# Performance work log

Hardware: AMD Instinct MI355X
Metric: run time of the kernel (lower is better)

## Reference

```python
import jax, jax.numpy as jnp
import numpy as np

B, T, D, H = 4, 2048, 1024, 16
HD = D // H  # 64
EPS = 1e-5

def _layernorm(x, g, b):
    mu = jnp.mean(x, axis=-1, keepdims=True)
    var = jnp.var(x, axis=-1, keepdims=True)
    return (x - mu) * jax.lax.rsqrt(var + EPS) * g + b

def setup_inputs() -> dict:
    key = jax.random.key(0)
    ks = jax.random.split(key, 8)
    s = D ** -0.5
    return {
        "x":  jax.random.normal(ks[0], (B, T, D), jnp.float32),
        "Wq": jax.random.normal(ks[1], (H, D, HD), jnp.float32) * s,
        "Wk": jax.random.normal(ks[2], (H, D, HD), jnp.float32) * s,
        "Wv": jax.random.normal(ks[3], (H, D, HD), jnp.float32) * s,
        "Wp": jax.random.normal(ks[4], (D, D), jnp.float32) * s,
        "bp": jnp.zeros((D,), jnp.float32),
        "W1": jax.random.normal(ks[5], (D, 4 * D), jnp.float32) * s,
        "b1": jnp.zeros((4 * D,), jnp.float32),
        "W2": jax.random.normal(ks[6], (4 * D, D), jnp.float32) * (4 * D) ** -0.5,
        "b2": jnp.zeros((D,), jnp.float32),
        "g1": jnp.ones((D,), jnp.float32),
        "be1": jnp.zeros((D,), jnp.float32),
        "g2": jnp.ones((D,), jnp.float32),
        "be2": jnp.zeros((D,), jnp.float32),
    }

def reference(x, Wq, Wk, Wv, Wp, bp, W1, b1, W2, b2, g1, be1, g2, be2):
    # --- pre-LN causal MHA (all heads batched; torch code loops per head) ---
    h = _layernorm(x, g1, be1)                       # [B,T,D]
    q = jnp.einsum('btd,hdk->bhtk', h, Wq)
    k = jnp.einsum('btd,hdk->bhtk', h, Wk)
    v = jnp.einsum('btd,hdk->bhtk', h, Wv)
    scores = jnp.einsum('bhtk,bhsk->bhts', q, k) * (HD ** -0.5)
    causal = jnp.tril(jnp.ones((T, T), bool))
    scores = jnp.where(causal, scores, -jnp.inf)
    w = jax.nn.softmax(scores, axis=-1)              # [B,H,T,T]
    o = jnp.einsum('bhts,bhsk->bhtk', w, v)          # [B,H,T,HD]
    o = o.transpose(0, 2, 1, 3).reshape(x.shape[0], x.shape[1], D)  # concat heads
    x = x + o @ Wp + bp                              # residual 1
    # --- pre-LN FFN ---
    h2 = _layernorm(x, g2, be2)
    ff = jax.nn.relu(h2 @ W1 + b1) @ W2 + b2
    return x + ff
```

## Files before the change

kernel.cpp:

```cpp
#include <hip/hip_runtime.h>
#include <hip/hip_bf16.h>
#include <math.h>

#define Bsz 4
#define Tsz 2048
#define Dsz 1024
#define Hn  16
#define HDs 64

typedef __attribute__((ext_vector_type(8))) short bf16x8;
typedef __attribute__((ext_vector_type(4))) float f32x4;

typedef const __attribute__((address_space(1))) void gvoid;
typedef __attribute__((address_space(3))) void lvoid;

__device__ __forceinline__ void async_copy16(const short* g, short* l) {
    __builtin_amdgcn_global_load_lds((gvoid*)g, (lvoid*)l, 16, 0, 0);
}

__device__ __forceinline__ short f2bf(float x) {
    __hip_bfloat16 h = __float2bfloat16(x);
    return *reinterpret_cast<short*>(&h);
}

__device__ __forceinline__ unsigned int pack_bf16(float hi, float lo) {
    unsigned int uh = __float_as_uint(hi) + 0x8000u;
    unsigned int ul = __float_as_uint(lo) + 0x8000u;
    return __builtin_amdgcn_perm(uh, ul, 0x07060302u);
}

__device__ __forceinline__ size_t headed_idx(int m, int c) {
    int b = m >> 11, t = m & 2047, h = c >> 6, kc = c & 63;
    return (((size_t)(b * Hn + h) * Tsz + t) << 6) + kc;
}

__global__ __launch_bounds__(256) void ln_kernel(const float* __restrict__ x,
                                                 const float* __restrict__ g,
                                                 const float* __restrict__ beta,
                                                 short* __restrict__ out)
{
    const int row = blockIdx.x;
    const float* xr = x + (size_t)row * Dsz;
    float v[4];
    float s = 0.f, s2 = 0.f;
#pragma unroll
    for (int i = 0; i < 4; ++i) {
        v[i] = xr[threadIdx.x + 256 * i];
        s += v[i];
        s2 += v[i] * v[i];
    }
#pragma unroll
    for (int off = 32; off; off >>= 1) {
        s  += __shfl_xor(s,  off);
        s2 += __shfl_xor(s2, off);
    }
    __shared__ float red[8];
    const int wave = threadIdx.x >> 6;
    if ((threadIdx.x & 63) == 0) { red[wave * 2] = s; red[wave * 2 + 1] = s2; }
    __syncthreads();
    s  = red[0] + red[2] + red[4] + red[6];
    s2 = red[1] + red[3] + red[5] + red[7];
    const float mu  = s * (1.f / Dsz);
    const float var = s2 * (1.f / Dsz) - mu * mu;
    const float rs  = rsqrtf(var + 1e-5f);
    short* orow = out + (size_t)row * Dsz;
#pragma unroll
    for (int i = 0; i < 4; ++i) {
        int col = threadIdx.x + 256 * i;
        orow[col] = f2bf((v[i] - mu) * rs * g[col] + beta[col]);
    }
}

__global__ __launch_bounds__(256) void transpose_cvt(
    const float* __restrict__ in, short* __restrict__ outp, int R, int C)
{
    __shared__ float tile[32][33];
    const int r0 = blockIdx.y * 32, c0 = blockIdx.x * 32;
    const size_t so = (size_t)blockIdx.z * R * C;
    const int tx = threadIdx.x & 31, ty = threadIdx.x >> 5;
    const float* ip = in + so;
    short* op = outp + so;
#pragma unroll
    for (int i = 0; i < 4; ++i)
        tile[ty + i * 8][tx] = ip[(size_t)(r0 + ty + i * 8) * C + c0 + tx];
    __syncthreads();
#pragma unroll
    for (int i = 0; i < 4; ++i)
        op[(size_t)(c0 + ty + i * 8) * R + r0 + tx] = f2bf(tile[tx][ty + i * 8]);
}

__global__ __launch_bounds__(256) void transpose_cvt_qkv(
    const float* __restrict__ Wq, const float* __restrict__ Wk,
    const float* __restrict__ Wv, short* __restrict__ outp)
{
    __shared__ float tile[32][33];
    const int z = blockIdx.z;
    const float* in = (z < 16) ? Wq : (z < 32) ? Wk : Wv;
    const int zz = z & 15;
    const int r0 = blockIdx.y * 32, c0 = blockIdx.x * 32;
    const int tx = threadIdx.x & 31, ty = threadIdx.x >> 5;
    const float* ip = in + (size_t)zz * (1024 * 64);
    short* op = outp + (size_t)z * (1024 * 64);
#pragma unroll
    for (int i = 0; i < 4; ++i)
        tile[ty + i * 8][tx] = ip[(size_t)(r0 + ty + i * 8) * 64 + c0 + tx];
    __syncthreads();
#pragma unroll
    for (int i = 0; i < 4; ++i)
        op[(size_t)(c0 + ty + i * 8) * 1024 + r0 + tx] = f2bf(tile[tx][ty + i * 8]);
}

template <int EPI>
__global__ __launch_bounds__(256) void gemm_mfma(
    const short* __restrict__ A, const short* __restrict__ Bt,
    const float* __restrict__ bias, const float* __restrict__ resid,
    float* __restrict__ Cf, short* __restrict__ Cb0,
    short* __restrict__ Cb1, short* __restrict__ Cb2,
    int M, int N, int K, float scale)
{
    __shared__ short As[2][128 * 32];
    __shared__ short Bs[2][128 * 32];
    const int tid  = threadIdx.x;
    const int lane = tid & 63, wave = tid >> 6;
    const int quad = lane >> 4, l16 = lane & 15;

    const int lin = blockIdx.y * gridDim.x + blockIdx.x;
    const int xcd = lin & 7;
    const int s   = lin >> 3;
    const int my  = xcd * 8 + (s & 7);
    const int nx  = s >> 3;
    const int m0 = my * 128, n0 = nx * 128;

    const int wm = (wave >> 1) * 64, wn = (wave & 1) * 64;

    f32x4 acc[4][4];
#pragma unroll
    for (int i = 0; i < 4; ++i)
#pragma unroll
        for (int j = 0; j < 4; ++j) acc[i][j] = f32x4{0.f, 0.f, 0.f, 0.f};

    const short* gA = A  + (size_t)(m0 + wave * 32 + (lane >> 2)) * K + (lane & 3) * 8;
    const short* gB = Bt + (size_t)(n0 + wave * 32 + (lane >> 2)) * K + (lane & 3) * 8;
    const size_t rstep = (size_t)16 * K;
    const int woff = wave * 1024;

    auto stageg = [&](int buf) {
        async_copy16(gA,         &As[buf][woff]);
        async_copy16(gA + rstep, &As[buf][woff + 512]);
        async_copy16(gB,         &Bs[buf][woff]);
        async_copy16(gB + rstep, &Bs[buf][woff + 512]);
        gA += 32; gB += 32;
    };

    stageg(0);
    stageg(1);

    const int ntile = K >> 5;
    int cur = 0;
    for (int t = 0; t < ntile; ++t) {
        if (t + 1 < ntile) asm volatile("s_waitcnt vmcnt(4)" ::: "memory");
        else               asm volatile("s_waitcnt vmcnt(0)" ::: "memory");
        __builtin_amdgcn_s_barrier();
        __builtin_amdgcn_sched_barrier(0);

        bf16x8 af[4], bfr[4];
#pragma unroll
        for (int mt = 0; mt < 4; ++mt)
            af[mt] = *(const bf16x8*)(&As[cur][(wm + mt * 16 + l16) * 32 + quad * 8]);
#pragma unroll
        for (int nt2 = 0; nt2 < 4; ++nt2)
            bfr[nt2] = *(const bf16x8*)(&Bs[cur][(wn + nt2 * 16 + l16) * 32 + quad * 8]);

        if (t + 2 < ntile) {
            asm volatile("s_waitcnt lgkmcnt(0)" ::: "memory");
            __builtin_amdgcn_sched_barrier(0);
            __builtin_amdgcn_s_barrier();
            __builtin_amdgcn_sched_barrier(0);
            stageg(cur);
        }

#pragma unroll
        for (int mt = 0; mt < 4; ++mt)
#pragma unroll
            for (int nt2 = 0; nt2 < 4; ++nt2)
                acc[mt][nt2] = __builtin_amdgcn_mfma_f32_16x16x32_bf16(
                    af[mt], bfr[nt2], acc[mt][nt2], 0, 0, 0);
        cur ^= 1;
    }

#pragma unroll
    for (int mt = 0; mt < 4; ++mt) {
#pragma unroll
        for (int nt2 = 0; nt2 < 4; ++nt2) {
#pragma unroll
            for (int r = 0; r < 4; ++r) {
                const int m = m0 + wm + mt * 16 + quad * 4 + r;
                const int c = n0 + wn + nt2 * 16 + l16;
                float val = acc[mt][nt2][r];
                if (EPI == 0) {
                    const int sel = c >> 10, cl = c & 1023;
                    if (sel == 0)
                        Cb0[headed_idx(m, cl)] = f2bf(val * scale);
                    else if (sel == 1)
                        Cb1[headed_idx(m, cl)] = f2bf(val);
                    else {
                        int b = m >> 11, t = m & 2047;
                        size_t idx = ((((size_t)((b << 4) | (cl >> 6)) << 6) | (cl & 63)) << 11) | t;
                        Cb2[idx] = f2bf(val);
                    }
                } else if (EPI == 2) {
                    size_t idx = (size_t)m * N + c;
                    Cf[idx] = val + bias[c] + resid[idx];
                } else {
                    float v2 = val + bias[c];
                    Cb0[(size_t)m * N + c] = f2bf(v2 > 0.f ? v2 : 0.f);
                }
            }
        }
    }
}

__global__ __launch_bounds__(256) void gemm_n64(
    const short* __restrict__ A, const short* __restrict__ Bt,
    const float* __restrict__ bias, const float* __restrict__ resid,
    float* __restrict__ Cf, int M, int N, int K)
{
    __shared__ short As[2][128 * 64];
    __shared__ short Bs[2][64 * 64];
    const int tid  = threadIdx.x;
    const int lane = tid & 63, wave = tid >> 6;
    const int quad = lane >> 4, l16 = lane & 15;

    const int lin = blockIdx.y * 16 + blockIdx.x;
    const int xcd = lin & 7;
    const int s   = lin >> 3;
    const int m0  = (xcd * 8 + (s & 7)) * 128;
    const int n0  = (s >> 3) * 64;

    const int wm = (wave >> 1) * 64, wn = (wave & 1) * 32;

    f32x4 acc[4][2];
#pragma unroll
    for (int i = 0; i < 4; ++i)
#pragma unroll
        for (int j = 0; j < 2; ++j) acc[i][j] = f32x4{0.f, 0.f, 0.f, 0.f};

    const short* gA[4];
    const short* gB[2];
    int dA[4], dB[2];
#pragma unroll
    for (int i = 0; i < 4; ++i) {
        const int sl = tid + 256 * i, r = sl >> 3, g = (sl & 7) ^ (r & 7);
        gA[i] = A + (size_t)(m0 + r) * K + g * 8;
        dA[i] = sl * 8;
    }
#pragma unroll
    for (int i = 0; i < 2; ++i) {
        const int sl = tid + 256 * i, r = sl >> 3, g = (sl & 7) ^ (r & 7);
        gB[i] = Bt + (size_t)(n0 + r) * K + g * 8;
        dB[i] = sl * 8;
    }

    auto stageg = [&](int buf) {
#pragma unroll
        for (int i = 0; i < 4; ++i) { async_copy16(gA[i], &As[buf][dA[i]]); gA[i] += 64; }
#pragma unroll
        for (int i = 0; i < 2; ++i) { async_copy16(gB[i], &Bs[buf][dB[i]]); gB[i] += 64; }
    };

    stageg(0);
    stageg(1);

    const int ntile = K >> 6;
    int cur = 0;
    for (int t = 0; t < ntile; ++t) {
        if (t + 1 < ntile) asm volatile("s_waitcnt vmcnt(6)" ::: "memory");
        else               asm volatile("s_waitcnt vmcnt(0)" ::: "memory");
        __builtin_amdgcn_s_barrier();
        __builtin_amdgcn_sched_barrier(0);

        bf16x8 af[4][2], bfr[2][2];
#pragma unroll
        for (int mt = 0; mt < 4; ++mt) {
            const int r = wm + mt * 16 + l16;
            af[mt][0] = *(const bf16x8*)(&As[cur][r * 64 + (((quad    ) ^ (r & 7)) << 3)]);
            af[mt][1] = *(const bf16x8*)(&As[cur][r * 64 + (((quad + 4) ^ (r & 7)) << 3)]);
        }
#pragma unroll
        for (int nt2 = 0; nt2 < 2; ++nt2) {
            const int r = wn + nt2 * 16 + l16;
            bfr[nt2][0] = *(const bf16x8*)(&Bs[cur][r * 64 + (((quad    ) ^ (r & 7)) << 3)]);
            bfr[nt2][1] = *(const bf16x8*)(&Bs[cur][r * 64 + (((quad + 4) ^ (r & 7)) << 3)]);
        }

        if (t + 2 < ntile) {
            asm volatile("s_waitcnt lgkmcnt(0)" ::: "memory");
            __builtin_amdgcn_sched_barrier(0);
            __builtin_amdgcn_s_barrier();
            __builtin_amdgcn_sched_barrier(0);
            stageg(cur);
        }

#pragma unroll
        for (int mt = 0; mt < 4; ++mt)
#pragma unroll
            for (int nt2 = 0; nt2 < 2; ++nt2) {
                acc[mt][nt2] = __builtin_amdgcn_mfma_f32_16x16x32_bf16(
                    af[mt][0], bfr[nt2][0], acc[mt][nt2], 0, 0, 0);
                acc[mt][nt2] = __builtin_amdgcn_mfma_f32_16x16x32_bf16(
                    af[mt][1], bfr[nt2][1], acc[mt][nt2], 0, 0, 0);
            }
        cur ^= 1;
    }

#pragma unroll
    for (int mt = 0; mt < 4; ++mt) {
#pragma unroll
        for (int nt2 = 0; nt2 < 2; ++nt2) {
#pragma unroll
            for (int r = 0; r < 4; ++r) {
                const int m = m0 + wm + mt * 16 + quad * 4 + r;
                const int c = n0 + wn + nt2 * 16 + l16;
                const size_t idx = (size_t)m * N + c;
                Cf[idx] = acc[mt][nt2][r] + bias[c] + resid[idx];
            }
        }
    }
}

__global__ __launch_bounds__(256, 4) void fattn_kernel(
    const short* __restrict__ Q,
    const short* __restrict__ K,
    const short* __restrict__ VT,
    short* __restrict__ O)
{
    __shared__ short Kl[2][64 * 64];
    __shared__ short Vl[2][64 * 64];
    __shared__ short p_lds[4][16 * 64];
    const int tid  = threadIdx.x;
    const int lane = tid & 63, wave = tid >> 6;
    const int quad = lane >> 4, l16 = lane & 15;

    const int lin  = blockIdx.y * 16 + blockIdx.x;
    const int xcd  = lin & 7;
    const int slot = lin >> 3;
    const int bh   = xcd * 8 + (slot >> 4);
    const int px   = slot & 15;
    const int tiles[2] = { 31 - px, px };

    const int bb = bh >> 4, hh = bh & 15;
    const size_t bhoff = (size_t)bh * (Tsz * HDs);
    const short* Qb = Q + bhoff;
    const short* Kb = K + bhoff;
    const short* Vb = VT + bhoff;

    const int s_a = tid, s_b = tid + 256;
    const int ra = s_a >> 3, ga = (s_a & 7) ^ (ra & 7);
    const int rb = s_b >> 3, gb = (s_b & 7) ^ (rb & 7);

    short* pw = &p_lds[wave][0];
    const int rd0 = l16 * 64 + (((quad    ) ^ (l16 & 7)) << 3);
    const int rd1 = l16 * 64 + (((quad + 4) ^ (l16 & 7)) << 3);

    bf16x8 bq[2][2];
#pragma unroll
    for (int ti = 0; ti < 2; ++ti) {
        const short* qp = Qb + (size_t)(tiles[ti] * 64 + wave * 16 + l16) * 64 + quad * 8;
        bq[ti][0] = *(const bf16x8*)qp;
        bq[ti][1] = *(const bf16x8*)(qp + 32);
    }

    auto stage = [&](int c64, int buf) {
        short* kb_l = &Kl[buf][0];
        short* vb_l = &Vl[buf][0];
        async_copy16(Kb + (((size_t)(c64 + ra)) << 6) + (ga << 3), kb_l + s_a * 8);
        async_copy16(Kb + (((size_t)(c64 + rb)) << 6) + (gb << 3), kb_l + s_b * 8);
        async_copy16(Vb + ((size_t)ra << 11) + c64 + (ga << 3), vb_l + s_a * 8);
        async_copy16(Vb + ((size_t)rb << 11) + c64 + (gb << 3), vb_l + s_b * 8);
    };

    stage(tiles[0] * 0, 0);
    __syncthreads();

    int phase = 0;
#pragma unroll
    for (int ti = 0; ti < 2; ++ti) {
        const int tile = tiles[ti];
        const int q0w  = tile * 64 + wave * 16;
        const int nch  = tile + 1;

        f32x4 oaccT[4];
        float lacc = 0.f;
#pragma unroll
        for (int nt = 0; nt < 4; ++nt) oaccT[nt] = f32x4{0.f, 0.f, 0.f, 0.f};

        for (int c = 0; c < nch; ++c) {
            const int cur = phase & 1;
            if (c + 1 < nch)   stage((c + 1) * 64, cur ^ 1);
            else if (ti == 0)  stage(0, cur ^ 1);

            const int s0 = c * 64;
            const short* Kc = &Kl[cur][0];
            const short* Vc = &Vl[cur][0];
            bf16x8 ak[4][2], av[4][2];
#pragma unroll
            for (int ct = 0; ct < 4; ++ct) {
                const int r = ct * 16 + l16;
                ak[ct][0] = *(const bf16x8*)(Kc + r * 64 + (((quad    ) ^ (r & 7)) << 3));
                ak[ct][1] = *(const bf16x8*)(Kc + r * 64 + (((quad + 4) ^ (r & 7)) << 3));
            }
#pragma unroll
            for (int nt = 0; nt < 4; ++nt) {
                const int r = nt * 16 + l16;
                av[nt][0] = *(const bf16x8*)(Vc + r * 64 + (((quad    ) ^ (r & 7)) << 3));
                av[nt][1] = *(const bf16x8*)(Vc + r * 64 + (((quad + 4) ^ (r & 7)) << 3));
            }
            f32x4 sfr[4];
#pragma unroll
            for (int ct = 0; ct < 4; ++ct) {
                f32x4 cc = {0.f, 0.f, 0.f, 0.f};
                cc = __builtin_amdgcn_mfma_f32_16x16x32_bf16(ak[ct][0], bq[ti][0], cc, 0, 0, 0);
                cc = __builtin_amdgcn_mfma_f32_16x16x32_bf16(ak[ct][1], bq[ti][1], cc, 0, 0, 0);
                sfr[ct] = cc;
            }
            if (s0 + 63 > q0w) {
                const int qr = q0w + l16;
#pragma unroll
                for (int ct = 0; ct < 4; ++ct)
#pragma unroll
                    for (int r = 0; r < 4; ++r)
                        if (s0 + ct * 16 + quad * 4 + r > qr)
                            sfr[ct][r] = -INFINITY;
            }
#pragma unroll
            for (int ct = 0; ct < 4; ++ct) {
                float p0 = __builtin_exp2f(sfr[ct][0]);
                float p1 = __builtin_exp2f(sfr[ct][1]);
                float p2 = __builtin_exp2f(sfr[ct][2]);
                float p3 = __builtin_exp2f(sfr[ct][3]);
                lacc += (p0 + p1) + (p2 + p3);
                uint2 pkv;
                pkv.x = pack_bf16(p1, p0);
                pkv.y = pack_bf16(p3, p2);
                const int g = (2 * ct + (quad >> 1)) ^ (l16 & 7);
                *(uint2*)(pw + l16 * 64 + (g << 3) + (quad & 1) * 4) = pkv;
            }
            bf16x8 bp0 = *(const bf16x8*)(pw + rd0);
            bf16x8 bp1 = *(const bf16x8*)(pw + rd1);
#pragma unroll
            for (int nt = 0; nt < 4; ++nt) {
                oaccT[nt] = __builtin_amdgcn_mfma_f32_16x16x32_bf16(av[nt][0], bp0, oaccT[nt], 0, 0, 0);
                oaccT[nt] = __builtin_amdgcn_mfma_f32_16x16x32_bf16(av[nt][1], bp1, oaccT[nt], 0, 0, 0);
            }
            __syncthreads();
            ++phase;
        }

        float ps = lacc;
        ps += __shfl_xor(ps, 16);
        ps += __shfl_xor(ps, 32);
        const float inv = 1.f / ps;
        short* orow = O + (size_t)(bb * Tsz + q0w + l16) * Dsz + hh * 64;
#pragma unroll
        for (int nt = 0; nt < 4; ++nt) {
            uint2 pkv;
            pkv.x = pack_bf16(oaccT[nt][1] * inv, oaccT[nt][0] * inv);
            pkv.y = pack_bf16(oaccT[nt][3] * inv, oaccT[nt][2] * inv);
            *(uint2*)(orow + nt * 16 + quad * 4) = pkv;
        }
    }
}

extern "C" void kernel_launch(void* const* d_in, const int* in_sizes, int n_in,
                              void* d_out, int out_size, void* d_ws, size_t ws_size,
                              hipStream_t stream) {
    const float* x   = (const float*)d_in[0];
    const float* Wq  = (const float*)d_in[1];
    const float* Wk  = (const float*)d_in[2];
    const float* Wv  = (const float*)d_in[3];
    const float* Wp  = (const float*)d_in[4];
    const float* bp  = (const float*)d_in[5];
    const float* W1  = (const float*)d_in[6];
    const float* b1  = (const float*)d_in[7];
    const float* W2  = (const float*)d_in[8];
    const float* b2  = (const float*)d_in[9];
    const float* g1  = (const float*)d_in[10];
    const float* be1 = (const float*)d_in[11];
    const float* g2  = (const float*)d_in[12];
    const float* be2 = (const float*)d_in[13];
    float* out = (float*)d_out;
    char*  W   = (char*)d_ws;

    short* h1  = (short*)(W);
    short* ff1 = (short*)(W);
    short* qb  = (short*)(W + (16ull << 20));
    short* kb  = (short*)(W + (32ull << 20));
    short* vtb = (short*)(W + (48ull << 20));
    short* o   = (short*)(W + (64ull << 20));
    short* h2  = (short*)(W + (80ull << 20));
    short* wqt = (short*)(W + (96ull << 20));
    short* wpt = (short*)(W + (102ull << 20));
    short* w1t = (short*)(W + (104ull << 20));
    short* w2t = (short*)(W + (112ull << 20));

    const int M = Bsz * Tsz;
    const float qscale = 0.125f * 1.44269504f;

    transpose_cvt_qkv<<<dim3(2, 32, 48), 256, 0, stream>>>(Wq, Wk, Wv, wqt);
    transpose_cvt<<<dim3(32, 32, 1),  256, 0, stream>>>(Wp, wpt, 1024, 1024);
    transpose_cvt<<<dim3(128, 32, 1), 256, 0, stream>>>(W1, w1t, 1024, 4096);
    transpose_cvt<<<dim3(32, 128, 1), 256, 0, stream>>>(W2, w2t, 4096, 1024);

    ln_kernel<<<dim3(M), 256, 0, stream>>>(x, g1, be1, h1);

    gemm_mfma<0><<<dim3(24, 64), 256, 0, stream>>>(
        h1, wqt, nullptr, nullptr, nullptr, qb, kb, vtb, M, 3072, 1024, qscale);

    fattn_kernel<<<dim3(16, Bsz * Hn), 256, 0, stream>>>(qb, kb, vtb, o);

    gemm_n64<<<dim3(16, 64), 256, 0, stream>>>(
        o, wpt, bp, x, out, M, 1024, 1024);

    ln_kernel<<<dim3(M), 256, 0, stream>>>(out, g2, be2, h2);

    gemm_mfma<3><<<dim3(32, 64), 256, 0, stream>>>(
        h2, w1t, b1, nullptr, nullptr, ff1, nullptr, nullptr, M, 4096, 1024, 1.f);

    gemm_n64<<<dim3(16, 64), 256, 0, stream>>>(
        ff1, w2t, b2, out, out, M, 1024, 4096);
}
```

Measured before the change: 513.6 us.

## Add XOR-swizzled LDS layout and wide 128x256 GEMM tiles for QKV and FFN1

Gives the gemm_mfma LDS staging an XOR swizzle over pairs of rows so that fragment reads no longer hit the same banks. Replaces gemm_n64 with a gemm_wide kernel that uses 128x256 tiles (a 4x8 MFMA accumulator per wave) for the QKV and FFN1 projections, which increases reuse of the A operand. The N=1024 output projections now go through gemm_mfma<2> with 128x128 tiles. The wider tiles use more registers and leave fewer blocks in flight, which may reduce occupancy.

Measured after the change: 544.7 us. 6.1% more time.

```diff
diff --git a/kernel.cpp b/kernel.cpp
--- a/kernel.cpp
+++ b/kernel.cpp
@@ -139,10 +139,15 @@
 #pragma unroll
         for (int j = 0; j < 4; ++j) acc[i][j] = f32x4{0.f, 0.f, 0.f, 0.f};
 
-    const short* gA = A  + (size_t)(m0 + wave * 32 + (lane >> 2)) * K + (lane & 3) * 8;
-    const short* gB = Bt + (size_t)(n0 + wave * 32 + (lane >> 2)) * K + (lane & 3) * 8;
+    const int ssr = lane >> 3, sv = (lane & 7) ^ ssr;
+    const int srow = ssr * 2 + (sv >> 2), sgr = sv & 3;
+    const short* gA = A  + (size_t)(m0 + wave * 32 + srow) * K + sgr * 8;
+    const short* gB = Bt + (size_t)(n0 + wave * 32 + srow) * K + sgr * 8;
     const size_t rstep = (size_t)16 * K;
     const int woff = wave * 1024;
+
+    const int rofs = (l16 >> 1) * 64 +
+        (((((l16 & 1) << 2) | quad) ^ ((l16 >> 1) & 7)) << 3);
 
     auto stageg = [&](int buf) {
         async_copy16(gA,         &As[buf][woff]);
@@ -166,10 +171,10 @@
         bf16x8 af[4], bfr[4];
 #pragma unroll
         for (int mt = 0; mt < 4; ++mt)
-            af[mt] = *(const bf16x8*)(&As[cur][(wm + mt * 16 + l16) * 32 + quad * 8]);
+            af[mt] = *(const bf16x8*)(&As[cur][(wm + mt * 16) * 32 + rofs]);
 #pragma unroll
         for (int nt2 = 0; nt2 < 4; ++nt2)
-            bfr[nt2] = *(const bf16x8*)(&Bs[cur][(wn + nt2 * 16 + l16) * 32 + quad * 8]);
+            bfr[nt2] = *(const bf16x8*)(&Bs[cur][(wn + nt2 * 16) * 32 + rofs]);
 
         if (t + 2 < ntile) {
             asm volatile("s_waitcnt lgkmcnt(0)" ::: "memory");
@@ -220,58 +225,65 @@
     }
 }
 
-__global__ __launch_bounds__(256) void gemm_n64(
+template <int EPI>
+__global__ __launch_bounds__(256) void gemm_wide(
     const short* __restrict__ A, const short* __restrict__ Bt,
-    const float* __restrict__ bias, const float* __restrict__ resid,
-    float* __restrict__ Cf, int M, int N, int K)
+    const float* __restrict__ bias,
+    float* __restrict__ Cf, short* __restrict__ Cb0,
+    short* __restrict__ Cb1, short* __restrict__ Cb2,
+    int M, int N, int K, float scale)
 {
-    __shared__ short As[2][128 * 64];
-    __shared__ short Bs[2][64 * 64];
+    __shared__ short As[2][128 * 32];
+    __shared__ short Bs[2][256 * 32];
     const int tid  = threadIdx.x;
     const int lane = tid & 63, wave = tid >> 6;
     const int quad = lane >> 4, l16 = lane & 15;
 
-    const int lin = blockIdx.y * 16 + blockIdx.x;
+    const int lin = blockIdx.y * gridDim.x + blockIdx.x;
     const int xcd = lin & 7;
     const int s   = lin >> 3;
-    const int m0  = (xcd * 8 + (s & 7)) * 128;
-    const int n0  = (s >> 3) * 64;
-
-    const int wm = (wave >> 1) * 64, wn = (wave & 1) * 32;
-
-    f32x4 acc[4][2];
+    const int my  = xcd * 8 + (s & 7);
+    const int nx  = s >> 3;
+    const int m0 = my * 128, n0 = nx * 256;
+
+    const int wm = (wave >> 1) * 64, wn = (wave & 1) * 128;
+
+    f32x4 acc[4][8];
 #pragma unroll
     for (int i = 0; i < 4; ++i)
 #pragma unroll
-        for (int j = 0; j < 2; ++j) acc[i][j] = f32x4{0.f, 0.f, 0.f, 0.f};
-
-    const short* gA[4];
-    const short* gB[2];
-    int dA[4], dB[2];
+        for (int j = 0; j < 8; ++j) acc[i][j] = f32x4{0.f, 0.f, 0.f, 0.f};
+
+    const short* gAp[2];
+    const short* gBp[4];
+    int dA[2], dB[4];
+#pragma unroll
+    for (int i = 0; i < 2; ++i) {
+        const int sl = tid + 256 * i, sr = sl >> 3, v = (sl & 7) ^ (sr & 7);
+        gAp[i] = A + (size_t)(m0 + sr * 2 + (v >> 2)) * K + (v & 3) * 8;
+        dA[i] = sl * 8;
+    }
 #pragma unroll
     for (int i = 0; i < 4; ++i) {
-        const int sl = tid + 256 * i, r = sl >> 3, g = (sl & 7) ^ (r & 7);
-        gA[i] = A + (size_t)(m0 + r) * K + g * 8;
-        dA[i] = sl * 8;
-    }
-#pragma unroll
-    for (int i = 0; i < 2; ++i) {
-        const int sl = tid + 256 * i, r = sl >> 3, g = (sl & 7) ^ (r & 7);
-        gB[i] = Bt + (size_t)(n0 + r) * K + g * 8;
+        const int sl = tid + 256 * i, sr = sl >> 3, v = (sl & 7) ^ (sr & 7);
+        gBp[i] = Bt + (size_t)(n0 + sr * 2 + (v >> 2)) * K + (v & 3) * 8;
         dB[i] = sl * 8;
     }
 
+    const int rofs = (l16 >> 1) * 64 +
+        (((((l16 & 1) << 2) | quad) ^ ((l16 >> 1) & 7)) << 3);
+
     auto stageg = [&](int buf) {
 #pragma unroll
-        for (int i = 0; i < 4; ++i) { async_copy16(gA[i], &As[buf][dA[i]]); gA[i] += 64; }
-#pragma unroll
-        for (int i = 0; i < 2; ++i) { async_copy16(gB[i], &Bs[buf][dB[i]]); gB[i] += 64; }
+        for (int i = 0; i < 2; ++i) { async_copy16(gAp[i], &As[buf][dA[i]]); gAp[i] += 32; }
+#pragma unroll
+        for (int i = 0; i < 4; ++i) { async_copy16(gBp[i], &Bs[buf][dB[i]]); gBp[i] += 32; }
     };
 
     stageg(0);
     stageg(1);
 
-    const int ntile = K >> 6;
+    const int ntile = K >> 5;
     int cur = 0;
     for (int t = 0; t < ntile; ++t) {
         if (t + 1 < ntile) asm volatile("s_waitcnt vmcnt(6)" ::: "memory");
@@ -279,19 +291,13 @@
         __builtin_amdgcn_s_barrier();
         __builtin_amdgcn_sched_barrier(0);
 
-        bf16x8 af[4][2], bfr[2][2];
-#pragma unroll
-        for (int mt = 0; mt < 4; ++mt) {
-            const int r = wm + mt * 16 + l16;
-            af[mt][0] = *(const bf16x8*)(&As[cur][r * 64 + (((quad    ) ^ (r & 7)) << 3)]);
-            af[mt][1] = *(const bf16x8*)(&As[cur][r * 64 + (((quad + 4) ^ (r & 7)) << 3)]);
-        }
-#pragma unroll
-        for (int nt2 = 0; nt2 < 2; ++nt2) {
-            const int r = wn + nt2 * 16 + l16;
-            bfr[nt2][0] = *(const bf16x8*)(&Bs[cur][r * 64 + (((quad    ) ^ (r & 7)) << 3)]);
-            bfr[nt2][1] = *(const bf16x8*)(&Bs[cur][r * 64 + (((quad + 4) ^ (r & 7)) << 3)]);
-        }
+        bf16x8 af[4], bfr[8];
+#pragma unroll
+        for (int mt = 0; mt < 4; ++mt)
+            af[mt] = *(const bf16x8*)(&As[cur][(wm + mt * 16) * 32 + rofs]);
+#pragma unroll
+        for (int nt2 = 0; nt2 < 8; ++nt2)
+            bfr[nt2] = *(const bf16x8*)(&Bs[cur][(wn + nt2 * 16) * 32 + rofs]);
 
         if (t + 2 < ntile) {
             asm volatile("s_waitcnt lgkmcnt(0)" ::: "memory");
@@ -304,25 +310,36 @@
 #pragma unroll
         for (int mt = 0; mt < 4; ++mt)
 #pragma unroll
-            for (int nt2 = 0; nt2 < 2; ++nt2) {
+            for (int nt2 = 0; nt2 < 8; ++nt2)
                 acc[mt][nt2] = __builtin_amdgcn_mfma_f32_16x16x32_bf16(
-                    af[mt][0], bfr[nt2][0], acc[mt][nt2], 0, 0, 0);
-                acc[mt][nt2] = __builtin_amdgcn_mfma_f32_16x16x32_bf16(
-                    af[mt][1], bfr[nt2][1], acc[mt][nt2], 0, 0, 0);
-            }
+                    af[mt], bfr[nt2], acc[mt][nt2], 0, 0, 0);
         cur ^= 1;
     }
 
 #pragma unroll
     for (int mt = 0; mt < 4; ++mt) {
 #pragma unroll
-        for (int nt2 = 0; nt2 < 2; ++nt2) {
+        for (int nt2 = 0; nt2 < 8; ++nt2) {
 #pragma unroll
             for (int r = 0; r < 4; ++r) {
                 const int m = m0 + wm + mt * 16 + quad * 4 + r;
                 const int c = n0 + wn + nt2 * 16 + l16;
-                const size_t idx = (size_t)m * N + c;
-                Cf[idx] = acc[mt][nt2][r] + bias[c] + resid[idx];
+                float val = acc[mt][nt2][r];
+                if (EPI == 0) {
+                    const int sel = c >> 10, cl = c & 1023;
+                    if (sel == 0)
+                        Cb0[headed_idx(m, cl)] = f2bf(val * scale);
+                    else if (sel == 1)
+                        Cb1[headed_idx(m, cl)] = f2bf(val);
+                    else {
+                        int b = m >> 11, t = m & 2047;
+                        size_t idx = ((((size_t)((b << 4) | (cl >> 6)) << 6) | (cl & 63)) << 11) | t;
+                        Cb2[idx] = f2bf(val);
+                    }
+                } else {
+                    float v2 = val + bias[c];
+                    Cb0[(size_t)m * N + c] = f2bf(v2 > 0.f ? v2 : 0.f);
+                }
             }
         }
     }
@@ -513,19 +530,19 @@
 
     ln_kernel<<<dim3(M), 256, 0, stream>>>(x, g1, be1, h1);
 
-    gemm_mfma<0><<<dim3(24, 64), 256, 0, stream>>>(
-        h1, wqt, nullptr, nullptr, nullptr, qb, kb, vtb, M, 3072, 1024, qscale);
+    gemm_wide<0><<<dim3(12, 64), 256, 0, stream>>>(
+        h1, wqt, nullptr, nullptr, qb, kb, vtb, M, 3072, 1024, qscale);
 
     fattn_kernel<<<dim3(16, Bsz * Hn), 256, 0, stream>>>(qb, kb, vtb, o);
 
-    gemm_n64<<<dim3(16, 64), 256, 0, stream>>>(
-        o, wpt, bp, x, out, M, 1024, 1024);
+    gemm_mfma<2><<<dim3(8, 64), 256, 0, stream>>>(
+        o, wpt, bp, x, out, nullptr, nullptr, nullptr, M, 1024, 1024, 1.f);
 
     ln_kernel<<<dim3(M), 256, 0, stream>>>(out, g2, be2, h2);
 
-    gemm_mfma<3><<<dim3(32, 64), 256, 0, stream>>>(
-        h2, w1t, b1, nullptr, nullptr, ff1, nullptr, nullptr, M, 4096, 1024, 1.f);
-
-    gemm_n64<<<dim3(16, 64), 256, 0, stream>>>(
-        ff1, w2t, b2, out, out, M, 1024, 4096);
-}
+    gemm_wide<3><<<dim3(16, 64), 256, 0, stream>>>(
+        h2, w1t, b1, nullptr, ff1, nullptr, nullptr, M, 4096, 1024, 1.f);
+
+    gemm_mfma<2><<<dim3(8, 64), 256, 0, stream>>>(
+        ff1, w2t, b2, out, out, nullptr, nullptr, nullptr, M, 1024, 4096, 1.f);
+}
```
